# Performance work log

Hardware: AMD Instinct MI355X
Metric: run time of the kernel (lower is better)

Reference implementation:

```python
import jax, jax.numpy as jnp
import numpy as np

N, E = 100000, 1600000
IN_C, HID, OUT_C = 128, 16, 32
H1, H2 = 8, 8  # heads for conv1/conv2; conv3 has 1 head, concat=False
NEG_SLOPE = 0.2


def setup_inputs() -> dict:
    key = jax.random.key(0)
    ks = jax.random.split(key, 16)
    def p(k, shape, fan_in):
        return jax.random.normal(k, shape, jnp.float32) * (1.0 / np.sqrt(fan_in))
    inp = {
        "x": jax.random.normal(ks[0], (N, IN_C), jnp.float32),
        "edge_index": jax.random.randint(ks[1], (2, E), 0, N, jnp.int32),
        # conv1: in=128 -> heads=8, ch=16, concat
        "W1": p(ks[2], (IN_C, H1 * HID), IN_C),
        "a_src1": p(ks[3], (H1, HID), HID),
        "a_dst1": p(ks[4], (H1, HID), HID),
        "b1": jnp.zeros((H1 * HID,), jnp.float32),
        # conv2: in=128 -> heads=8, ch=16, concat
        "W2": p(ks[5], (H1 * HID, H2 * HID), H1 * HID),
        "a_src2": p(ks[6], (H2, HID), HID),
        "a_dst2": p(ks[7], (H2, HID), HID),
        "b2": jnp.zeros((H2 * HID,), jnp.float32),
        # conv3: in=128 -> heads=1, ch=32, concat=False
        "W3": p(ks[8], (H2 * HID, OUT_C), H2 * HID),
        "a_src3": p(ks[9], (1, OUT_C), OUT_C),
        "a_dst3": p(ks[10], (1, OUT_C), OUT_C),
        "b3": jnp.zeros((OUT_C,), jnp.float32),
    }
    return inp


def gat_conv(x, src, dst, W, a_src, a_dst, b, heads, ch, concat):
    """PyG-style GATConv (eval mode): gather -> leaky_relu -> segment softmax -> scatter sum."""
    n = x.shape[0]
    h = (x @ W).reshape(n, heads, ch)                 # [N, H, C]
    al_s = jnp.sum(h * a_src, axis=-1)                # [N, H] source-side logit part
    al_d = jnp.sum(h * a_dst, axis=-1)                # [N, H] dest-side logit part
    logits = jax.nn.leaky_relu(al_s[src] + al_d[dst], NEG_SLOPE)  # [Etot, H]
    m = jax.ops.segment_max(logits, dst, num_segments=n)         # per-dest max (self loops guarantee >=1 edge)
    e = jnp.exp(logits - m[dst])
    denom = jax.ops.segment_sum(e, dst, num_segments=n)
    alpha = e / denom[dst]                            # [Etot, H]
    msgs = h[src] * alpha[..., None]                  # [Etot, H, C]
    out = jax.ops.segment_sum(msgs, dst, num_segments=n)  # [N, H, C]
    if concat:
        return out.reshape(n, heads * ch) + b
    return out.mean(axis=1) + b


def reference(x, edge_index, W1, a_src1, a_dst1, b1, W2, a_src2, a_dst2, b2,
              W3, a_src3, a_dst3, b3):
    n = x.shape[0]
    loops = jnp.arange(n, dtype=edge_index.dtype)     # PyG add_self_loops=True
    src = jnp.concatenate([edge_index[0], loops])
    dst = jnp.concatenate([edge_index[1], loops])
    h = jax.nn.relu(gat_conv(x, src, dst, W1, a_src1, a_dst1, b1, H1, HID, True))
    h = jax.nn.relu(gat_conv(h, src, dst, W2, a_src2, a_dst2, b2, H2, HID, True))
    h = gat_conv(h, src, dst, W3, a_src3, a_dst3, b3, 1, OUT_C, False)
    # global_mean_pool with all-zero batch vector -> mean over all nodes
    return h.mean(axis=0, keepdims=True)              # [1, OUT_C]
```

## Files before the change

### kernel.cpp

```cpp
#include <hip/hip_runtime.h>


typedef unsigned short bfu;
typedef unsigned char u8;
typedef __attribute__((ext_vector_type(8))) short bf16x8;
typedef __attribute__((ext_vector_type(4))) float f32x4;
typedef __attribute__((ext_vector_type(2))) float f32x2;
typedef __attribute__((ext_vector_type(4))) int i32x4;

constexpr int N_NODES = 100000;
constexpr int E_IN    = 1600000;
constexpr int E_TOT   = E_IN + N_NODES;
constexpr float NEG   = 0.2f;
constexpr int P_XCD   = 8;
constexpr int PSZ     = N_NODES / P_XCD;
constexpr int CAP     = 48;
constexpr int AGG32_B = N_NODES / 32;
constexpr int AGG128_B = N_NODES / 32;
constexpr int GEMM_B  = (N_NODES + 63) / 64;
constexpr int EDGE_B4 = (E_TOT / 4 + 255) / 256;
constexpr int FILL_B  = EDGE_B4 * P_XCD;
constexpr int TW_B    = (36864 + 255) / 256;

__device__ inline bfu f2bf(float f) {
    union { float f; unsigned i; } c; c.f = f;
    unsigned x = c.i;
    return (bfu)((x + 0x7fffu + ((x >> 16) & 1u)) >> 16);
}
__device__ inline u8 f2fp8(float f) {
    return (u8)(__builtin_amdgcn_cvt_pk_fp8_f32(f, f, 0, false) & 0xff);
}


__device__ inline void fill_body(int g, int tid, const int* __restrict__ ei,
                                 int* __restrict__ cursor, int* __restrict__ srclist) {
    int p = g & 7;
    int b = g >> 3;
    int lo = p * PSZ;
    int e0 = (b * 256 + tid) * 4;
    if (e0 >= E_TOT) return;
    bool self = e0 >= E_IN;
    i32x4 d4;
    if (!self) d4 = __builtin_nontemporal_load((const i32x4*)(ei + E_IN + e0));
    else { int bb = e0 - E_IN; d4 = (i32x4){bb, bb + 1, bb + 2, bb + 3}; }
    #pragma unroll
    for (int q = 0; q < 4; ++q) {
        int d = d4[q];
        if ((unsigned)(d - lo) < (unsigned)PSZ) {
            int s = self ? (e0 - E_IN + q) : __builtin_nontemporal_load(ei + e0 + q);
            int pos = atomicAdd(&cursor[d], 1);
            if (pos < CAP) srclist[d * CAP + pos] = s;
        }
    }
}

__global__ __launch_bounds__(256) void fill_w(const int* __restrict__ ei,
        int* __restrict__ cursor, int* __restrict__ srclist,
        const float* __restrict__ W1, const float* __restrict__ W2,
        const float* __restrict__ W3, bfu* __restrict__ Wt1,
        bfu* __restrict__ Wt2, bfu* __restrict__ Wt3) {
    if (blockIdx.x < FILL_B) {
        fill_body(blockIdx.x, threadIdx.x, ei, cursor, srclist);
        return;
    }
    int idx = (blockIdx.x - FILL_B) * 256 + threadIdx.x;
    if (idx < 16384) {
        int k = idx >> 7, n = idx & 127;
        Wt1[n * 128 + k] = f2bf(W1[idx]);
    } else if (idx < 32768) {
        int r = idx - 16384;
        int k = r >> 7, n = r & 127;
        Wt2[n * 128 + k] = f2bf(W2[r]);
    } else if (idx < 36864) {
        int r = idx - 32768;
        int k = r >> 5, n = r & 31;
        Wt3[n * 128 + k] = f2bf(W3[r]);
    }
}


__device__ inline bf16x8 ldcvt_f32(const float* p) {
    float4 v0 = *(const float4*)p;
    float4 v1 = *(const float4*)(p + 4);
    bf16x8 a;
    a[0] = (short)f2bf(v0.x); a[1] = (short)f2bf(v0.y);
    a[2] = (short)f2bf(v0.z); a[3] = (short)f2bf(v0.w);
    a[4] = (short)f2bf(v1.x); a[5] = (short)f2bf(v1.y);
    a[6] = (short)f2bf(v1.z); a[7] = (short)f2bf(v1.w);
    return a;
}

template<int COUT, bool F32A, int H>
__global__ __launch_bounds__(256) void gemm_mfma(const void* __restrict__ Xg_,
                                                 const bfu* __restrict__ Wt,
                                                 const float* __restrict__ a_src,
                                                 const float* __restrict__ a_dst,
                                                 u8* __restrict__ Y,
                                                 float* __restrict__ als,
                                                 float* __restrict__ ald) {
    constexpr int NT = COUT / 16;
    int wid  = threadIdx.x >> 6;
    int lane = threadIdx.x & 63;
    int m = lane & 15, quad = lane >> 4;
    int rbase = (blockIdx.x * 4 + wid) * 16;
    if (rbase >= N_NODES) return;
    int rA = rbase + m; if (rA >= N_NODES) rA = N_NODES - 1;

    bf16x8 a0, a1, a2, a3;
    if constexpr (F32A) {
        const float* Ap = (const float*)Xg_ + (size_t)rA * 128 + quad * 8;
        a0 = ldcvt_f32(Ap);
        a1 = ldcvt_f32(Ap + 32);
        a2 = ldcvt_f32(Ap + 64);
        a3 = ldcvt_f32(Ap + 96);
    } else {
        const bfu* Ap = (const bfu*)Xg_ + (size_t)rA * 128 + quad * 8;
        a0 = *(const bf16x8*)(Ap);
        a1 = *(const bf16x8*)(Ap + 32);
        a2 = *(const bf16x8*)(Ap + 64);
        a3 = *(const bf16x8*)(Ap + 96);
    }

    const bfu* Bp = Wt + (size_t)m * 128 + quad * 8;
    f32x4 acc[NT];
    #pragma unroll
    for (int nt = 0; nt < NT; nt++) {
        const bfu* Bn = Bp + nt * 16 * 128;
        f32x4 c = {0.f, 0.f, 0.f, 0.f};
        c = __builtin_amdgcn_mfma_f32_16x16x32_bf16(a0, *(const bf16x8*)(Bn),      c, 0, 0, 0);
        c = __builtin_amdgcn_mfma_f32_16x16x32_bf16(a1, *(const bf16x8*)(Bn + 32), c, 0, 0, 0);
        c = __builtin_amdgcn_mfma_f32_16x16x32_bf16(a2, *(const bf16x8*)(Bn + 64), c, 0, 0, 0);
        c = __builtin_amdgcn_mfma_f32_16x16x32_bf16(a3, *(const bf16x8*)(Bn + 96), c, 0, 0, 0);
        acc[nt] = c;
    }

    #pragma unroll
    for (int nt = 0; nt < NT; nt++) {
        #pragma unroll
        for (int r = 0; r < 4; r++) {
            int row = rbase + quad * 4 + r;
            if (row < N_NODES)
                Y[(size_t)row * COUT + nt * 16 + m] = f2fp8(acc[nt][r]);
        }
    }

    if constexpr (H == 8) {
        #pragma unroll
        for (int nt = 0; nt < NT; nt++) {
            float as_ = a_src[nt * 16 + m];
            float ad_ = a_dst[nt * 16 + m];
            #pragma unroll
            for (int r = 0; r < 4; r++) {
                float vs = acc[nt][r] * as_;
                float vd = acc[nt][r] * ad_;
                #pragma unroll
                for (int mask = 1; mask < 16; mask <<= 1) {
                    vs += __shfl_xor(vs, mask);
                    vd += __shfl_xor(vd, mask);
                }
                int row = rbase + quad * 4 + r;
                if (m == 0 && row < N_NODES) {
                    als[row * 8 + nt] = vs;
                    ald[row * 8 + nt] = vd;
                }
            }
        }
    } else {
        float as0 = a_src[m], as1 = a_src[16 + m];
        float ad0 = a_dst[m], ad1 = a_dst[16 + m];
        #pragma unroll
        for (int r = 0; r < 4; r++) {
            float vs = acc[0][r] * as0 + acc[1][r] * as1;
            float vd = acc[0][r] * ad0 + acc[1][r] * ad1;
            #pragma unroll
            for (int mask = 1; mask < 16; mask <<= 1) {
                vs += __shfl_xor(vs, mask);
                vd += __shfl_xor(vd, mask);
            }
            int row = rbase + quad * 4 + r;
            if (m == 0 && row < N_NODES) {
                als[row] = vs;
                ald[row] = vd;
            }
        }
    }
}


__device__ inline void unpack_fma(uint4 u, float w, float* a) {
    f32x2 p;
    p = __builtin_amdgcn_cvt_pk_f32_fp8((int)u.x, false); a[0]=fmaf(w,p[0],a[0]);  a[1]=fmaf(w,p[1],a[1]);
    p = __builtin_amdgcn_cvt_pk_f32_fp8((int)u.x, true);  a[2]=fmaf(w,p[0],a[2]);  a[3]=fmaf(w,p[1],a[3]);
    p = __builtin_amdgcn_cvt_pk_f32_fp8((int)u.y, false); a[4]=fmaf(w,p[0],a[4]);  a[5]=fmaf(w,p[1],a[5]);
    p = __builtin_amdgcn_cvt_pk_f32_fp8((int)u.y, true);  a[6]=fmaf(w,p[0],a[6]);  a[7]=fmaf(w,p[1],a[7]);
    p = __builtin_amdgcn_cvt_pk_f32_fp8((int)u.z, false); a[8]=fmaf(w,p[0],a[8]);  a[9]=fmaf(w,p[1],a[9]);
    p = __builtin_amdgcn_cvt_pk_f32_fp8((int)u.z, true);  a[10]=fmaf(w,p[0],a[10]); a[11]=fmaf(w,p[1],a[11]);
    p = __builtin_amdgcn_cvt_pk_f32_fp8((int)u.w, false); a[12]=fmaf(w,p[0],a[12]); a[13]=fmaf(w,p[1],a[13]);
    p = __builtin_amdgcn_cvt_pk_f32_fp8((int)u.w, true);  a[14]=fmaf(w,p[0],a[14]); a[15]=fmaf(w,p[1],a[15]);
}

__global__ __launch_bounds__(256) void agg128(const u8* __restrict__ Hb,
        const float* __restrict__ als, const float* __restrict__ ald,
        const int* __restrict__ deg, const int* __restrict__ srclist,
        const float* __restrict__ bias, bfu* __restrict__ out) {
    int wave = blockIdx.x * 4 + (threadIdx.x >> 6);
    int lane = threadIdx.x & 63;
    int sub  = lane >> 3;
    int li   = lane & 7;
    int d    = wave * 8 + sub;
    int c0   = li * 16;
    float ad = ald[d * 8 + li];
    const int* sl = srclist + d * CAP;
    int n = deg[d]; n = n < CAP ? n : CAP;
    float a[16];
    #pragma unroll
    for (int k = 0; k < 16; ++k) a[k] = 0.f;
    float den = 0.f;
    int j = 0;
    for (; j + 2 <= n; j += 2) {
        int s0 = sl[j], s1 = sl[j + 1];
        uint4 u0 = *(const uint4*)(Hb + (size_t)s0 * 128 + c0);
        uint4 u1 = *(const uint4*)(Hb + (size_t)s1 * 128 + c0);
        float x0 = als[s0 * 8 + li], x1 = als[s1 * 8 + li];
        float l0 = x0 + ad; l0 = fmaxf(l0, NEG * l0); float w0 = __expf(l0);
        float l1 = x1 + ad; l1 = fmaxf(l1, NEG * l1); float w1 = __expf(l1);
        den += w0 + w1;
        unpack_fma(u0, w0, a);
        unpack_fma(u1, w1, a);
    }
    if (j < n) {
        int s0 = sl[j];
        uint4 u0 = *(const uint4*)(Hb + (size_t)s0 * 128 + c0);
        float x0 = als[s0 * 8 + li];
        float l0 = x0 + ad; l0 = fmaxf(l0, NEG * l0); float w0 = __expf(l0);
        den += w0;
        unpack_fma(u0, w0, a);
    }
    float r = 1.f / den;
    unsigned dw[8];
    #pragma unroll
    for (int k = 0; k < 8; ++k) {
        float e0 = fmaxf(fmaf(a[2*k],   r, bias[c0 + 2*k]),   0.f);
        float e1 = fmaxf(fmaf(a[2*k+1], r, bias[c0 + 2*k+1]), 0.f);
        dw[k] = (unsigned)f2bf(e0) | ((unsigned)f2bf(e1) << 16);
    }
    uint4 st0 = {dw[0], dw[1], dw[2], dw[3]};
    uint4 st1 = {dw[4], dw[5], dw[6], dw[7]};
    *(uint4*)&out[(size_t)d * 128 + c0]     = st0;
    *(uint4*)&out[(size_t)d * 128 + c0 + 8] = st1;
}

__global__ __launch_bounds__(256) void agg32(const u8* __restrict__ Hb,
        const float* __restrict__ als, const float* __restrict__ ald,
        const int* __restrict__ deg, const int* __restrict__ srclist,
        const float* __restrict__ bias, float* __restrict__ outp) {
    __shared__ float lds[4][32];
    int t    = threadIdx.x;
    int wid  = t >> 6;
    int lane = t & 63;
    int sub  = lane >> 3;
    int li   = lane & 7;
    int d    = blockIdx.x * 32 + wid * 8 + sub;
    int c0 = li * 4;
    float adv = ald[d];
    const int* sl = srclist + d * CAP;
    int n = deg[d]; n = n < CAP ? n : CAP;
    float a0=0.f,a1=0.f,a2=0.f,a3=0.f,den=0.f;
    int j = 0;
    for (; j + 4 <= n; j += 4) {
        int s0 = sl[j], s1 = sl[j+1], s2 = sl[j+2], s3 = sl[j+3];
        unsigned u0 = *(const unsigned*)(Hb + (size_t)s0 * 32 + c0);
        unsigned u1 = *(const unsigned*)(Hb + (size_t)s1 * 32 + c0);
        unsigned u2 = *(const unsigned*)(Hb + (size_t)s2 * 32 + c0);
        unsigned u3 = *(const unsigned*)(Hb + (size_t)s3 * 32 + c0);
        float x0 = als[s0], x1 = als[s1], x2 = als[s2], x3 = als[s3];
        float l0 = x0 + adv; l0 = fmaxf(l0, NEG*l0); float w0 = __expf(l0);
        float l1 = x1 + adv; l1 = fmaxf(l1, NEG*l1); float w1 = __expf(l1);
        float l2 = x2 + adv; l2 = fmaxf(l2, NEG*l2); float w2 = __expf(l2);
        float l3 = x3 + adv; l3 = fmaxf(l3, NEG*l3); float w3 = __expf(l3);
        den += (w0 + w1) + (w2 + w3);
        f32x2 p;
        p = __builtin_amdgcn_cvt_pk_f32_fp8((int)u0, false); a0=fmaf(w0,p[0],a0); a1=fmaf(w0,p[1],a1);
        p = __builtin_amdgcn_cvt_pk_f32_fp8((int)u0, true);  a2=fmaf(w0,p[0],a2); a3=fmaf(w0,p[1],a3);
        p = __builtin_amdgcn_cvt_pk_f32_fp8((int)u1, false); a0=fmaf(w1,p[0],a0); a1=fmaf(w1,p[1],a1);
        p = __builtin_amdgcn_cvt_pk_f32_fp8((int)u1, true);  a2=fmaf(w1,p[0],a2); a3=fmaf(w1,p[1],a3);
        p = __builtin_amdgcn_cvt_pk_f32_fp8((int)u2, false); a0=fmaf(w2,p[0],a0); a1=fmaf(w2,p[1],a1);
        p = __builtin_amdgcn_cvt_pk_f32_fp8((int)u2, true);  a2=fmaf(w2,p[0],a2); a3=fmaf(w2,p[1],a3);
        p = __builtin_amdgcn_cvt_pk_f32_fp8((int)u3, false); a0=fmaf(w3,p[0],a0); a1=fmaf(w3,p[1],a1);
        p = __builtin_amdgcn_cvt_pk_f32_fp8((int)u3, true);  a2=fmaf(w3,p[0],a2); a3=fmaf(w3,p[1],a3);
    }
    for (; j < n; ++j) {
        int s0 = sl[j];
        unsigned u0 = *(const unsigned*)(Hb + (size_t)s0 * 32 + c0);
        float x0 = als[s0];
        float l0 = x0 + adv; l0 = fmaxf(l0, NEG*l0); float w0 = __expf(l0);
        den += w0;
        f32x2 p;
        p = __builtin_amdgcn_cvt_pk_f32_fp8((int)u0, false); a0=fmaf(w0,p[0],a0); a1=fmaf(w0,p[1],a1);
        p = __builtin_amdgcn_cvt_pk_f32_fp8((int)u0, true);  a2=fmaf(w0,p[0],a2); a3=fmaf(w0,p[1],a3);
    }
    float r = 1.f / den;
    float4 bv = *(const float4*)&bias[c0];
    float o0 = fmaf(a0, r, bv.x), o1 = fmaf(a1, r, bv.y);
    float o2 = fmaf(a2, r, bv.z), o3 = fmaf(a3, r, bv.w);
    #pragma unroll
    for (int mask = 8; mask < 64; mask <<= 1) {
        o0 += __shfl_xor(o0, mask);
        o1 += __shfl_xor(o1, mask);
        o2 += __shfl_xor(o2, mask);
        o3 += __shfl_xor(o3, mask);
    }
    if (sub == 0) {
        lds[wid][c0]     = o0;
        lds[wid][c0 + 1] = o1;
        lds[wid][c0 + 2] = o2;
        lds[wid][c0 + 3] = o3;
    }
    __syncthreads();
    if (t < 32)
        atomicAdd(&outp[t],
            (lds[0][t] + lds[1][t] + lds[2][t] + lds[3][t]) * (1.0f / N_NODES));
}


extern "C" void kernel_launch(void* const* d_in, const int* in_sizes, int n_in,
                              void* d_out, int out_size, void* d_ws, size_t ws_size,
                              hipStream_t stream) {
    (void)in_sizes; (void)n_in; (void)out_size; (void)ws_size;
    const float* x   = (const float*)d_in[0];
    const int*   ei  = (const int*)d_in[1];
    const float* W1  = (const float*)d_in[2];
    const float* as1 = (const float*)d_in[3];
    const float* ad1 = (const float*)d_in[4];
    const float* b1  = (const float*)d_in[5];
    const float* W2  = (const float*)d_in[6];
    const float* as2 = (const float*)d_in[7];
    const float* ad2 = (const float*)d_in[8];
    const float* b2  = (const float*)d_in[9];
    const float* W3  = (const float*)d_in[10];
    const float* as3 = (const float*)d_in[11];
    const float* ad3 = (const float*)d_in[12];
    const float* b3  = (const float*)d_in[13];

    char* ws = (char*)d_ws;
    size_t off = 0;
    auto carve = [&](size_t bytes) { void* p = ws + off; off += (bytes + 255) & ~size_t(255); return p; };
    u8*    bufH    = (u8*)carve(size_t(N_NODES) * 128);
    bfu*   bufF    = (bfu*)carve(size_t(N_NODES) * 128 * 2);
    float* als     = (float*)carve(size_t(N_NODES) * 8 * 4);
    float* ald     = (float*)carve(size_t(N_NODES) * 8 * 4);
    int*   cursor  = (int*)carve(size_t(N_NODES) * 4);
    bfu*   Wt1     = (bfu*)carve(128 * 128 * 2);
    bfu*   Wt2     = (bfu*)carve(128 * 128 * 2);
    bfu*   Wt3     = (bfu*)carve(32 * 128 * 2);
    int*   srclist = (int*)carve(size_t(N_NODES) * CAP * 4);

    hipMemsetAsync(cursor, 0, size_t(N_NODES) * 4, stream);
    hipMemsetAsync(d_out, 0, 32 * 4, stream);

    fill_w<<<FILL_B + TW_B, 256, 0, stream>>>(ei, cursor, srclist,
                                              W1, W2, W3, Wt1, Wt2, Wt3);

    gemm_mfma<128, true, 8><<<GEMM_B, 256, 0, stream>>>(x, Wt1, as1, ad1, bufH, als, ald);
    agg128<<<AGG128_B, 256, 0, stream>>>(bufH, als, ald, cursor, srclist, b1, bufF);

    gemm_mfma<128, false, 8><<<GEMM_B, 256, 0, stream>>>(bufF, Wt2, as2, ad2, bufH, als, ald);
    agg128<<<AGG128_B, 256, 0, stream>>>(bufH, als, ald, cursor, srclist, b2, bufF);

    gemm_mfma<32, false, 1><<<GEMM_B, 256, 0, stream>>>(bufF, Wt3, as3, ad3, bufH, als, ald);
    agg32<<<AGG32_B, 256, 0, stream>>>(bufH, als, ald, cursor, srclist, b3, (float*)d_out);
}
```

Measured before the change: 470.0 us.

## Bin edges by destination partition before CSR-style scatter

```diff
diff --git a/kernel.cpp b/kernel.cpp
--- a/kernel.cpp
+++ b/kernel.cpp
@@ -10,7 +10,6 @@
 
 constexpr int N_NODES = 100000;
 constexpr int E_IN    = 1600000;
-constexpr int E_TOT   = E_IN + N_NODES;
 constexpr float NEG   = 0.2f;
 constexpr int P_XCD   = 8;
 constexpr int PSZ     = N_NODES / P_XCD;
@@ -18,9 +17,13 @@
 constexpr int AGG32_B = N_NODES / 32;
 constexpr int AGG128_B = N_NODES / 32;
 constexpr int GEMM_B  = (N_NODES + 63) / 64;
-constexpr int EDGE_B4 = (E_TOT / 4 + 255) / 256;
-constexpr int FILL_B  = EDGE_B4 * P_XCD;
+constexpr int BIN_B   = (E_IN / 4 + 255) / 256;
 constexpr int TW_B    = (36864 + 255) / 256;
+constexpr int BINCAP  = 272;
+constexpr int BCAP    = 231424;
+constexpr int MBLK    = BCAP / 1024;
+constexpr int SELF_B  = 13;
+constexpr int SCAT_B  = P_XCD * (MBLK + SELF_B);
 
 __device__ inline bfu f2bf(float f) {
     union { float f; unsigned i; } c; c.f = f;
@@ -32,49 +35,95 @@
 }
 
 
-__device__ inline void fill_body(int g, int tid, const int* __restrict__ ei,
-                                 int* __restrict__ cursor, int* __restrict__ srclist) {
-    int p = g & 7;
-    int b = g >> 3;
-    int lo = p * PSZ;
-    int e0 = (b * 256 + tid) * 4;
-    if (e0 >= E_TOT) return;
-    bool self = e0 >= E_IN;
-    i32x4 d4;
-    if (!self) d4 = __builtin_nontemporal_load((const i32x4*)(ei + E_IN + e0));
-    else { int bb = e0 - E_IN; d4 = (i32x4){bb, bb + 1, bb + 2, bb + 3}; }
-    #pragma unroll
-    for (int q = 0; q < 4; ++q) {
-        int d = d4[q];
-        if ((unsigned)(d - lo) < (unsigned)PSZ) {
-            int s = self ? (e0 - E_IN + q) : __builtin_nontemporal_load(ei + e0 + q);
-            int pos = atomicAdd(&cursor[d], 1);
-            if (pos < CAP) srclist[d * CAP + pos] = s;
-        }
-    }
-}
-
-__global__ __launch_bounds__(256) void fill_w(const int* __restrict__ ei,
-        int* __restrict__ cursor, int* __restrict__ srclist,
+__global__ __launch_bounds__(256) void bin_w(const int* __restrict__ ei,
+        uint2* __restrict__ gbkt, int* __restrict__ gcount,
         const float* __restrict__ W1, const float* __restrict__ W2,
         const float* __restrict__ W3, bfu* __restrict__ Wt1,
         bfu* __restrict__ Wt2, bfu* __restrict__ Wt3) {
-    if (blockIdx.x < FILL_B) {
-        fill_body(blockIdx.x, threadIdx.x, ei, cursor, srclist);
+    if (blockIdx.x >= BIN_B) {
+        int idx = (blockIdx.x - BIN_B) * 256 + threadIdx.x;
+        if (idx < 16384) {
+            int k = idx >> 7, n = idx & 127;
+            Wt1[n * 128 + k] = f2bf(W1[idx]);
+        } else if (idx < 32768) {
+            int r = idx - 16384;
+            int k = r >> 7, n = r & 127;
+            Wt2[n * 128 + k] = f2bf(W2[r]);
+        } else if (idx < 36864) {
+            int r = idx - 32768;
+            int k = r >> 5, n = r & 31;
+            Wt3[n * 128 + k] = f2bf(W3[r]);
+        }
         return;
     }
-    int idx = (blockIdx.x - FILL_B) * 256 + threadIdx.x;
-    if (idx < 16384) {
-        int k = idx >> 7, n = idx & 127;
-        Wt1[n * 128 + k] = f2bf(W1[idx]);
-    } else if (idx < 32768) {
-        int r = idx - 16384;
-        int k = r >> 7, n = r & 127;
-        Wt2[n * 128 + k] = f2bf(W2[r]);
-    } else if (idx < 36864) {
-        int r = idx - 32768;
-        int k = r >> 5, n = r & 31;
-        Wt3[n * 128 + k] = f2bf(W3[r]);
+    __shared__ uint2 bins[8][BINCAP];
+    __shared__ int cnt[8];
+    __shared__ int base[8];
+    int tid = threadIdx.x;
+    if (tid < 8) cnt[tid] = 0;
+    __syncthreads();
+    int e0 = (blockIdx.x * 256 + tid) * 4;
+    if (e0 < E_IN) {
+        i32x4 s4 = *(const i32x4*)(ei + e0);
+        i32x4 d4 = *(const i32x4*)(ei + E_IN + e0);
+        #pragma unroll
+        for (int q = 0; q < 4; ++q) {
+            int d = d4[q], s = s4[q];
+            int p = (int)((unsigned)d / (unsigned)PSZ);
+            int pos = atomicAdd(&cnt[p], 1);
+            bins[p][pos] = make_uint2((unsigned)s, (unsigned)d);
+        }
+    }
+    __syncthreads();
+    if (tid < 8) base[tid] = atomicAdd(&gcount[tid], cnt[tid]);
+    __syncthreads();
+    #pragma unroll
+    for (int p = 0; p < 8; ++p) {
+        int c = cnt[p], b = base[p];
+        for (int i = tid; i < c; i += 256)
+            gbkt[(size_t)p * BCAP + b + i] = bins[p][i];
+    }
+}
+
+
+__global__ __launch_bounds__(256) void scatter(const uint2* __restrict__ gbkt,
+        const int* __restrict__ gcount, int* __restrict__ cursor,
+        int* __restrict__ srclist) {
+    int p = blockIdx.x & 7;
+    int b = blockIdx.x >> 3;
+    int tid = threadIdx.x;
+    if (b < MBLK) {
+        int cnt = gcount[p];
+        int i0 = b * 1024 + tid * 4;
+        if (i0 >= cnt) return;
+        const uint2* src = gbkt + (size_t)p * BCAP;
+        if (i0 + 4 <= cnt) {
+            uint4 u01 = *(const uint4*)(src + i0);
+            uint4 u23 = *(const uint4*)(src + i0 + 2);
+            int pos;
+            pos = atomicAdd(&cursor[u01.y], 1); if (pos < CAP) srclist[u01.y * CAP + pos] = (int)u01.x;
+            pos = atomicAdd(&cursor[u01.w], 1); if (pos < CAP) srclist[u01.w * CAP + pos] = (int)u01.z;
+            pos = atomicAdd(&cursor[u23.y], 1); if (pos < CAP) srclist[u23.y * CAP + pos] = (int)u23.x;
+            pos = atomicAdd(&cursor[u23.w], 1); if (pos < CAP) srclist[u23.w * CAP + pos] = (int)u23.z;
+        } else {
+            for (int i = i0; i < cnt; ++i) {
+                uint2 e = src[i];
+                int pos = atomicAdd(&cursor[e.y], 1);
+                if (pos < CAP) srclist[e.y * CAP + pos] = (int)e.x;
+            }
+        }
+    } else {
+        int bb = b - MBLK;
+        int n0 = p * PSZ + bb * 1024 + tid * 4;
+        int hi = (p + 1) * PSZ;
+        #pragma unroll
+        for (int q = 0; q < 4; ++q) {
+            int n = n0 + q;
+            if (n < hi) {
+                int pos = atomicAdd(&cursor[n], 1);
+                if (pos < CAP) srclist[n * CAP + pos] = n;
+            }
+        }
     }
 }
 
@@ -350,16 +399,19 @@
     float* als     = (float*)carve(size_t(N_NODES) * 8 * 4);
     float* ald     = (float*)carve(size_t(N_NODES) * 8 * 4);
     int*   cursor  = (int*)carve(size_t(N_NODES) * 4);
+    int*   gcount  = (int*)carve(8 * 4);
     bfu*   Wt1     = (bfu*)carve(128 * 128 * 2);
     bfu*   Wt2     = (bfu*)carve(128 * 128 * 2);
     bfu*   Wt3     = (bfu*)carve(32 * 128 * 2);
     int*   srclist = (int*)carve(size_t(N_NODES) * CAP * 4);
+    uint2* gbkt    = (uint2*)carve(size_t(P_XCD) * BCAP * 8);
 
     hipMemsetAsync(cursor, 0, size_t(N_NODES) * 4, stream);
+    hipMemsetAsync(gcount, 0, 8 * 4, stream);
     hipMemsetAsync(d_out, 0, 32 * 4, stream);
 
-    fill_w<<<FILL_B + TW_B, 256, 0, stream>>>(ei, cursor, srclist,
-                                              W1, W2, W3, Wt1, Wt2, Wt3);
+    bin_w<<<BIN_B + TW_B, 256, 0, stream>>>(ei, gbkt, gcount, W1, W2, W3, Wt1, Wt2, Wt3);
+    scatter<<<SCAT_B, 256, 0, stream>>>(gbkt, gcount, cursor, srclist);
 
     gemm_mfma<128, true, 8><<<GEMM_B, 256, 0, stream>>>(x, Wt1, as1, ad1, bufH, als, ald);
     agg128<<<AGG128_B, 256, 0, stream>>>(bufH, als, ald, cursor, srclist, b1, bufF);
```

Result: slower. 487.9 us (+3.8%).

## Fold attention vectors into extra GEMM columns and raise adjacency cap

Applied to the files above, without the earlier changes.

```diff
diff --git a/kernel.cpp b/kernel.cpp
--- a/kernel.cpp
+++ b/kernel.cpp
@@ -6,7 +6,6 @@
 typedef __attribute__((ext_vector_type(8))) short bf16x8;
 typedef __attribute__((ext_vector_type(4))) float f32x4;
 typedef __attribute__((ext_vector_type(2))) float f32x2;
-typedef __attribute__((ext_vector_type(4))) int i32x4;
 
 constexpr int N_NODES = 100000;
 constexpr int E_IN    = 1600000;
@@ -14,13 +13,14 @@
 constexpr float NEG   = 0.2f;
 constexpr int P_XCD   = 8;
 constexpr int PSZ     = N_NODES / P_XCD;
-constexpr int CAP     = 48;
+constexpr int CAP     = 64;
 constexpr int AGG32_B = N_NODES / 32;
 constexpr int AGG128_B = N_NODES / 32;
 constexpr int GEMM_B  = (N_NODES + 63) / 64;
 constexpr int EDGE_B4 = (E_TOT / 4 + 255) / 256;
 constexpr int FILL_B  = EDGE_B4 * P_XCD;
-constexpr int TW_B    = (36864 + 255) / 256;
+constexpr int PREP_ITEMS = 43008;
+constexpr int PREP_B  = (PREP_ITEMS + 255) / 256;
 
 __device__ inline bfu f2bf(float f) {
     union { float f; unsigned i; } c; c.f = f;
@@ -32,49 +32,87 @@
 }
 
 
-__device__ inline void fill_body(int g, int tid, const int* __restrict__ ei,
-                                 int* __restrict__ cursor, int* __restrict__ srclist) {
-    int p = g & 7;
-    int b = g >> 3;
-    int lo = p * PSZ;
-    int e0 = (b * 256 + tid) * 4;
+__device__ inline void prep_body(int idx,
+        const float* __restrict__ W1, const float* __restrict__ W2,
+        const float* __restrict__ W3,
+        const float* __restrict__ as1, const float* __restrict__ ad1,
+        const float* __restrict__ as2, const float* __restrict__ ad2,
+        const float* __restrict__ as3, const float* __restrict__ ad3,
+        bfu* __restrict__ WtX1, bfu* __restrict__ WtX2, bfu* __restrict__ WtX3) {
+    if (idx < 16384) {
+        int k = idx >> 7, n = idx & 127;
+        WtX1[n * 128 + k] = f2bf(W1[idx]);
+    } else if (idx < 32768) {
+        int r = idx - 16384;
+        int k = r >> 7, n = r & 127;
+        WtX2[n * 128 + k] = f2bf(W2[r]);
+    } else if (idx < 36864) {
+        int r = idx - 32768;
+        int k = r >> 5, n = r & 31;
+        WtX3[n * 128 + k] = f2bf(W3[r]);
+    } else if (idx < 38912) {
+        int r = idx - 36864;
+        int sd = r >> 10, rr = r & 1023;
+        int h = rr >> 7, k = rr & 127;
+        const float* a = sd ? ad1 : as1;
+        float v = 0.f;
+        #pragma unroll
+        for (int c = 0; c < 16; ++c) v += W1[k * 128 + h * 16 + c] * a[h * 16 + c];
+        WtX1[(128 + sd * 8 + h) * 128 + k] = f2bf(v);
+    } else if (idx < 40960) {
+        int r = idx - 38912;
+        int sd = r >> 10, rr = r & 1023;
+        int h = rr >> 7, k = rr & 127;
+        const float* a = sd ? ad2 : as2;
+        float v = 0.f;
+        #pragma unroll
+        for (int c = 0; c < 16; ++c) v += W2[k * 128 + h * 16 + c] * a[h * 16 + c];
+        WtX2[(128 + sd * 8 + h) * 128 + k] = f2bf(v);
+    } else if (idx < 41216) {
+        int r = idx - 40960;
+        int sd = r >> 7, k = r & 127;
+        const float* a = sd ? ad3 : as3;
+        float v = 0.f;
+        #pragma unroll
+        for (int c = 0; c < 32; ++c) v += W3[k * 32 + c] * a[c];
+        WtX3[(32 + sd) * 128 + k] = f2bf(v);
+    } else if (idx < 43008) {
+        WtX3[34 * 128 + (idx - 41216)] = 0;
+    }
+}
+
+
+__global__ __launch_bounds__(256) void fill_prep(const int* __restrict__ ei,
+        int* __restrict__ cursor, int* __restrict__ srclist,
+        const float* __restrict__ W1, const float* __restrict__ W2,
+        const float* __restrict__ W3,
+        const float* __restrict__ as1, const float* __restrict__ ad1,
+        const float* __restrict__ as2, const float* __restrict__ ad2,
+        const float* __restrict__ as3, const float* __restrict__ ad3,
+        bfu* __restrict__ WtX1, bfu* __restrict__ WtX2, bfu* __restrict__ WtX3) {
+    if (blockIdx.x >= FILL_B) {
+        int idx = (blockIdx.x - FILL_B) * 256 + threadIdx.x;
+        prep_body(idx, W1, W2, W3, as1, ad1, as2, ad2, as3, ad3, WtX1, WtX2, WtX3);
+        return;
+    }
+    int p = blockIdx.x & 7;
+    int b = blockIdx.x >> 3;
+    int lo = p * PSZ, hi = lo + PSZ;
+    int e0 = (b * 256 + threadIdx.x) * 4;
     if (e0 >= E_TOT) return;
     bool self = e0 >= E_IN;
-    i32x4 d4;
-    if (!self) d4 = __builtin_nontemporal_load((const i32x4*)(ei + E_IN + e0));
-    else { int bb = e0 - E_IN; d4 = (i32x4){bb, bb + 1, bb + 2, bb + 3}; }
+    int4 d4;
+    if (!self) d4 = *(const int4*)&ei[E_IN + e0];
+    else { int bb = e0 - E_IN; d4 = make_int4(bb, bb + 1, bb + 2, bb + 3); }
+    int dd[4] = {d4.x, d4.y, d4.z, d4.w};
     #pragma unroll
     for (int q = 0; q < 4; ++q) {
-        int d = d4[q];
-        if ((unsigned)(d - lo) < (unsigned)PSZ) {
-            int s = self ? (e0 - E_IN + q) : __builtin_nontemporal_load(ei + e0 + q);
+        int d = dd[q];
+        if (d >= lo && d < hi) {
+            int s = self ? (e0 - E_IN + q) : ei[e0 + q];
             int pos = atomicAdd(&cursor[d], 1);
             if (pos < CAP) srclist[d * CAP + pos] = s;
         }
-    }
-}
-
-__global__ __launch_bounds__(256) void fill_w(const int* __restrict__ ei,
-        int* __restrict__ cursor, int* __restrict__ srclist,
-        const float* __restrict__ W1, const float* __restrict__ W2,
-        const float* __restrict__ W3, bfu* __restrict__ Wt1,
-        bfu* __restrict__ Wt2, bfu* __restrict__ Wt3) {
-    if (blockIdx.x < FILL_B) {
-        fill_body(blockIdx.x, threadIdx.x, ei, cursor, srclist);
-        return;
-    }
-    int idx = (blockIdx.x - FILL_B) * 256 + threadIdx.x;
-    if (idx < 16384) {
-        int k = idx >> 7, n = idx & 127;
-        Wt1[n * 128 + k] = f2bf(W1[idx]);
-    } else if (idx < 32768) {
-        int r = idx - 16384;
-        int k = r >> 7, n = r & 127;
-        Wt2[n * 128 + k] = f2bf(W2[r]);
-    } else if (idx < 36864) {
-        int r = idx - 32768;
-        int k = r >> 5, n = r & 31;
-        Wt3[n * 128 + k] = f2bf(W3[r]);
     }
 }
 
@@ -90,15 +128,13 @@
     return a;
 }
 
-template<int COUT, bool F32A, int H>
+template<int NTO, bool F32A>
 __global__ __launch_bounds__(256) void gemm_mfma(const void* __restrict__ Xg_,
                                                  const bfu* __restrict__ Wt,
-                                                 const float* __restrict__ a_src,
-                                                 const float* __restrict__ a_dst,
                                                  u8* __restrict__ Y,
                                                  float* __restrict__ als,
                                                  float* __restrict__ ald) {
-    constexpr int NT = COUT / 16;
+    constexpr int COUT = NTO * 16;
     int wid  = threadIdx.x >> 6;
     int lane = threadIdx.x & 63;
     int m = lane & 15, quad = lane >> 4;
@@ -122,9 +158,9 @@
     }
 
     const bfu* Bp = Wt + (size_t)m * 128 + quad * 8;
-    f32x4 acc[NT];
-    #pragma unroll
-    for (int nt = 0; nt < NT; nt++) {
+    f32x4 acc[NTO + 1];
+    #pragma unroll
+    for (int nt = 0; nt <= NTO; nt++) {
         const bfu* Bn = Bp + nt * 16 * 128;
         f32x4 c = {0.f, 0.f, 0.f, 0.f};
         c = __builtin_amdgcn_mfma_f32_16x16x32_bf16(a0, *(const bf16x8*)(Bn),      c, 0, 0, 0);
@@ -135,7 +171,7 @@
     }
 
     #pragma unroll
-    for (int nt = 0; nt < NT; nt++) {
+    for (int nt = 0; nt < NTO; nt++) {
         #pragma unroll
         for (int r = 0; r < 4; r++) {
             int row = rbase + quad * 4 + r;
@@ -143,45 +179,17 @@
                 Y[(size_t)row * COUT + nt * 16 + m] = f2fp8(acc[nt][r]);
         }
     }
-
-    if constexpr (H == 8) {
-        #pragma unroll
-        for (int nt = 0; nt < NT; nt++) {
-            float as_ = a_src[nt * 16 + m];
-            float ad_ = a_dst[nt * 16 + m];
-            #pragma unroll
-            for (int r = 0; r < 4; r++) {
-                float vs = acc[nt][r] * as_;
-                float vd = acc[nt][r] * ad_;
-                #pragma unroll
-                for (int mask = 1; mask < 16; mask <<= 1) {
-                    vs += __shfl_xor(vs, mask);
-                    vd += __shfl_xor(vd, mask);
-                }
-                int row = rbase + quad * 4 + r;
-                if (m == 0 && row < N_NODES) {
-                    als[row * 8 + nt] = vs;
-                    ald[row * 8 + nt] = vd;
-                }
-            }
-        }
-    } else {
-        float as0 = a_src[m], as1 = a_src[16 + m];
-        float ad0 = a_dst[m], ad1 = a_dst[16 + m];
-        #pragma unroll
-        for (int r = 0; r < 4; r++) {
-            float vs = acc[0][r] * as0 + acc[1][r] * as1;
-            float vd = acc[0][r] * ad0 + acc[1][r] * ad1;
-            #pragma unroll
-            for (int mask = 1; mask < 16; mask <<= 1) {
-                vs += __shfl_xor(vs, mask);
-                vd += __shfl_xor(vd, mask);
-            }
-            int row = rbase + quad * 4 + r;
-            if (m == 0 && row < N_NODES) {
-                als[row] = vs;
-                ald[row] = vd;
-            }
+    #pragma unroll
+    for (int r = 0; r < 4; r++) {
+        int row = rbase + quad * 4 + r;
+        if (row >= N_NODES) continue;
+        float v = acc[NTO][r];
+        if constexpr (NTO == 8) {
+            if (m < 8) als[row * 8 + m] = v;
+            else       ald[row * 8 + (m - 8)] = v;
+        } else {
+            if (m == 0) als[row] = v;
+            else if (m == 1) ald[row] = v;
         }
     }
 }
@@ -350,23 +358,23 @@
     float* als     = (float*)carve(size_t(N_NODES) * 8 * 4);
     float* ald     = (float*)carve(size_t(N_NODES) * 8 * 4);
     int*   cursor  = (int*)carve(size_t(N_NODES) * 4);
-    bfu*   Wt1     = (bfu*)carve(128 * 128 * 2);
-    bfu*   Wt2     = (bfu*)carve(128 * 128 * 2);
-    bfu*   Wt3     = (bfu*)carve(32 * 128 * 2);
+    bfu*   WtX1    = (bfu*)carve(144 * 128 * 2);
+    bfu*   WtX2    = (bfu*)carve(144 * 128 * 2);
+    bfu*   WtX3    = (bfu*)carve(48 * 128 * 2);
     int*   srclist = (int*)carve(size_t(N_NODES) * CAP * 4);
 
     hipMemsetAsync(cursor, 0, size_t(N_NODES) * 4, stream);
     hipMemsetAsync(d_out, 0, 32 * 4, stream);
 
-    fill_w<<<FILL_B + TW_B, 256, 0, stream>>>(ei, cursor, srclist,
-                                              W1, W2, W3, Wt1, Wt2, Wt3);
-
-    gemm_mfma<128, true, 8><<<GEMM_B, 256, 0, stream>>>(x, Wt1, as1, ad1, bufH, als, ald);
+    fill_prep<<<FILL_B + PREP_B, 256, 0, stream>>>(ei, cursor, srclist,
+        W1, W2, W3, as1, ad1, as2, ad2, as3, ad3, WtX1, WtX2, WtX3);
+
+    gemm_mfma<8, true><<<GEMM_B, 256, 0, stream>>>(x, WtX1, bufH, als, ald);
     agg128<<<AGG128_B, 256, 0, stream>>>(bufH, als, ald, cursor, srclist, b1, bufF);
 
-    gemm_mfma<128, false, 8><<<GEMM_B, 256, 0, stream>>>(bufF, Wt2, as2, ad2, bufH, als, ald);
+    gemm_mfma<8, false><<<GEMM_B, 256, 0, stream>>>(bufF, WtX2, bufH, als, ald);
     agg128<<<AGG128_B, 256, 0, stream>>>(bufH, als, ald, cursor, srclist, b2, bufF);
 
-    gemm_mfma<32, false, 1><<<GEMM_B, 256, 0, stream>>>(bufF, Wt3, as3, ad3, bufH, als, ald);
+    gemm_mfma<2, false><<<GEMM_B, 256, 0, stream>>>(bufF, WtX3, bufH, als, ald);
     agg32<<<AGG32_B, 256, 0, stream>>>(bufH, als, ald, cursor, srclist, b3, (float*)d_out);
 }
```

Result: faster. 432.7 us (-7.9%).
